# Kernel optimization log

Hardware: AMD Instinct MI355X
Metric: run time of the kernel (lower is better)

## Reference

```python
import math
import jax, jax.numpy as jnp
import numpy as np

B, L, T, D, H, SD = 8, 512, 512, 768, 12, 5


def setup_inputs() -> dict:
    key = jax.random.key(0)
    ks = jax.random.split(key, 16)
    s = 0.02
    return {
        "q": jax.random.normal(ks[0], (B, L, D), jnp.float32),
        "k": jax.random.normal(ks[1], (B, T, D), jnp.float32),
        "v": jax.random.normal(ks[2], (B, T, D), jnp.float32),
        "pairwise_locs": jax.random.normal(ks[3], (B, L, T, SD), jnp.float32),
        "key_padding_mask": jax.random.randint(ks[4], (B, T), 0, 2).astype(bool),
        "Wq": jax.random.normal(ks[5], (D, D), jnp.float32) * s,
        "bq": jnp.zeros((D,), jnp.float32),
        "Wk": jax.random.normal(ks[6], (D, D), jnp.float32) * s,
        "bk": jnp.zeros((D,), jnp.float32),
        "Wv": jax.random.normal(ks[7], (D, D), jnp.float32) * s,
        "bv": jnp.zeros((D,), jnp.float32),
        "Wl": jax.random.normal(ks[8], (D, H * (SD + 1)), jnp.float32) * s,
        "bl": jnp.zeros((H * (SD + 1),), jnp.float32),
        "Wf": jax.random.normal(ks[9], (D, D), jnp.float32) * s,
        "bf": jnp.zeros((D,), jnp.float32),
    }


def reference(q, k, v, pairwise_locs, key_padding_mask,
              Wq, bq, Wk, bk, Wv, bv, Wl, bl, Wf, bf):
    b, l, d = q.shape
    t = k.shape[1]
    sd = pairwise_locs.shape[-1]
    h = Wl.shape[1] // (sd + 1)          # spatial_multihead=True -> h == n_head
    dh = d // h

    # projections -> [h, b, seq, dh]
    qh = (q @ Wq + bq).reshape(b, l, h, dh).transpose(2, 0, 1, 3)
    kh = (k @ Wk + bk).reshape(b, t, h, dh).transpose(2, 0, 1, 3)
    vh = (v @ Wv + bv).reshape(b, t, h, dh).transpose(2, 0, 1, 3)

    attn = jnp.einsum('hblk,hbtk->hblt', qh, kh) / math.sqrt(dh)

    # language-conditioned spatial weights from residual (= q input)
    sw = (q @ Wl + bl).reshape(b, l, h, sd + 1).transpose(2, 0, 1, 3)  # [h,b,l,sd+1]
    spatial_bias = sw[..., :1]
    spatial_w = sw[..., 1:]
    loc_attn = jax.nn.sigmoid(
        jnp.einsum('hbld,bltd->hblt', spatial_w, pairwise_locs) + spatial_bias)

    mask = key_padding_mask[None, :, None, :]          # [1,b,1,t]
    attn = jnp.where(mask, -jnp.inf, attn)
    loc_attn = jnp.where(mask, 0.0, loc_attn)

    fused_attn = jax.nn.softmax(jnp.log(jnp.clip(loc_attn, 1e-6)) + attn, axis=3)

    out = jnp.einsum('hblt,hbtv->hblv', fused_attn, vh)
    out = out.transpose(1, 2, 0, 3).reshape(b, l, d)
    out = out @ Wf + bf
    return (out, fused_attn)
```

## Files before the change

kernel.cpp:

```cpp
#include <hip/hip_runtime.h>
#include <hip/hip_bf16.h>

#define B_ 8
#define L_ 512
#define T_ 512
#define D_ 768
#define H_ 12
#define DH_ 64
#define SD_ 5
#define NSW_ 72
#define K2_ 1536
#define K3_ 2304

typedef __attribute__((ext_vector_type(8))) short bf16x8;
typedef __attribute__((ext_vector_type(4))) float f32x4;
typedef unsigned short ushort_t;

__device__ __forceinline__ unsigned short f2bf(float x) {
    union { __hip_bfloat16 h; unsigned short u; } cv;
    cv.h = __float2bfloat16(x);
    return cv.u;
}
__device__ __forceinline__ float bf2f(unsigned short u) {
    union { unsigned short u; __hip_bfloat16 h; } cv;
    cv.u = u;
    return __bfloat162float(cv.h);
}

__device__ __forceinline__ void gload_lds16(const void* g, void* l) {
    __builtin_amdgcn_global_load_lds((const __attribute__((address_space(1))) void*)g,
                                     (__attribute__((address_space(3))) void*)l,
                                     16, 0, 0);
}

__global__ __launch_bounds__(256) void asplit_kernel(
    const float* __restrict__ q, const float* __restrict__ k, const float* __restrict__ v,
    short* __restrict__ q2, short* __restrict__ k2, short* __restrict__ v2)
{
    const int z = blockIdx.z;
    const float* A = (z == 0) ? q : (z == 1) ? k : v;
    short* O = (z == 0) ? q2 : (z == 1) ? k2 : v2;
    const int col = blockIdx.x * 256 + threadIdx.x;
    const int m   = blockIdx.y;
    if (col >= D_) return;
    const float a = A[(size_t)m * D_ + col];
    const unsigned short hi = f2bf(a);
    const unsigned short lo = f2bf(a - bf2f(hi));
    O[(size_t)m * K2_ + col]       = (short)hi;
    O[(size_t)m * K2_ + D_ + col]  = (short)lo;
}

__global__ __launch_bounds__(256) void wsplit_kernel(
    const float* __restrict__ Wq, const float* __restrict__ Wk,
    const float* __restrict__ Wv, const float* __restrict__ Wl,
    const float* __restrict__ Wf,
    short* __restrict__ WqT3, short* __restrict__ WkT3, short* __restrict__ WvT3,
    short* __restrict__ WlT3, short* __restrict__ WfT3)
{
    const int z = blockIdx.z;
    const float* W; short* O; int Nw, Npad;
    if (z == 0)      { W = Wq; O = WqT3; Nw = D_;   Npad = 768; }
    else if (z == 1) { W = Wk; O = WkT3; Nw = D_;   Npad = 768; }
    else if (z == 2) { W = Wv; O = WvT3; Nw = D_;   Npad = 768; }
    else if (z == 3) { W = Wl; O = WlT3; Nw = NSW_; Npad = 128; }
    else             { W = Wf; O = WfT3; Nw = D_;   Npad = 768; }

    const int k0 = blockIdx.x * 64;
    const int n0 = blockIdx.y * 64;
    if (n0 >= Npad) return;

    __shared__ float sm[64][65];
    const int c  = threadIdx.x & 63;
    const int r4 = threadIdx.x >> 6;

#pragma unroll
    for (int i = 0; i < 16; i++) {
        const int r = i * 4 + r4;
        float val = 0.f;
        if (n0 + c < Nw) val = W[(size_t)(k0 + r) * Nw + n0 + c];
        sm[r][c] = val;
    }
    __syncthreads();

#pragma unroll
    for (int i = 0; i < 16; i++) {
        const int nl = i * 4 + r4;
        const int n  = n0 + nl;
        if (n >= Npad) continue;
        const float v = (n < Nw) ? sm[c][nl] : 0.f;
        const unsigned short hi = f2bf(v);
        const unsigned short lo = f2bf(v - bf2f(hi));
        const size_t rb = (size_t)n * K3_;
        O[rb + k0 + c]        = (short)hi;
        O[rb + 768 + k0 + c]  = (short)lo;
        O[rb + 1536 + k0 + c] = (short)hi;
    }
}

__global__ __launch_bounds__(256) void mfma_gemm(
    const short* __restrict__ q2, const short* __restrict__ k2, const short* __restrict__ v2,
    const short* __restrict__ WqT3, const short* __restrict__ WkT3,
    const short* __restrict__ WvT3, const short* __restrict__ WlT3,
    const short* __restrict__ WfT3,
    const float* __restrict__ bq, const float* __restrict__ bk,
    const float* __restrict__ bv, const float* __restrict__ bl,
    const float* __restrict__ bf,
    const short* __restrict__ outp2,
    ushort_t* __restrict__ qs2a, ushort_t* __restrict__ ks2a, ushort_t* __restrict__ vt2,
    float* __restrict__ swv, float* __restrict__ outf,
    int zoff)
{
    const int nwg   = gridDim.x * gridDim.y * gridDim.z;
    const int flat  = blockIdx.x + gridDim.x * (blockIdx.y + gridDim.y * blockIdx.z);
    const int flat2 = (flat & 7) * (nwg >> 3) + (flat >> 3);
    const int bxg   = flat2 % 6;
    const int rem   = flat2 / 6;
    const int byg   = rem & 31;
    const int bzg   = rem >> 5;

    const int z = zoff + bzg;
    const short* A2; const short* WT3; const float* bias;
    if (z == 0)      { A2 = q2;    WT3 = WqT3; bias = bq; }
    else if (z == 1) { A2 = k2;    WT3 = WkT3; bias = bk; }
    else if (z == 2) { A2 = v2;    WT3 = WvT3; bias = bv; }
    else if (z == 3) { A2 = q2;    WT3 = WlT3; bias = bl; }
    else             { A2 = outp2; WT3 = WfT3; bias = bf; }

    if (z == 3 && bxg != 0) return;

    const int m0 = byg * 128;
    const int n0 = bxg * 128;

    __shared__ __align__(16) short As[2][128 * 64];
    __shared__ __align__(16) short Bs[2][128 * 64];

    const int tid  = threadIdx.x;
    const int lane = tid & 63;
    const int wv_  = tid >> 6;
    const int wm   = (wv_ & 1) << 6;
    const int wn   = (wv_ >> 1) << 6;
    const int l15  = lane & 15;
    const int quad = lane >> 4;

    f32x4 acc[4][4] = {};

    const int NT = K3_ / 64;

    auto stage = [&](int buf, int kb) {
        const int akb = (kb < 768) ? kb : kb - 768;
#pragma unroll
        for (int j = 0; j < 4; j++) {
            const int i = tid + 256 * j;
            const int r = i >> 3, c = i & 7, gc = c ^ (r & 7);
            gload_lds16(A2 + (size_t)(m0 + r) * K2_ + akb + gc * 8, &As[buf][i * 8]);
        }
#pragma unroll
        for (int j = 0; j < 4; j++) {
            const int i = tid + 256 * j;
            const int r = i >> 3, c = i & 7, gc = c ^ (r & 7);
            gload_lds16(WT3 + (size_t)(n0 + r) * K3_ + kb + gc * 8, &Bs[buf][i * 8]);
        }
    };

    stage(0, 0);
    stage(1, 64);

    int cur = 0;
    for (int t = 0; t < NT; ++t) {
        asm volatile("s_waitcnt vmcnt(8)" ::: "memory");
        __builtin_amdgcn_s_barrier();

        bf16x8 af[2][4], bfr[2][4];
#pragma unroll
        for (int tt = 0; tt < 4; tt++) {
            const int ar = wm + tt * 16 + l15;
            const int br = wn + tt * 16 + l15;
            af[0][tt]  = *(const bf16x8*)&As[cur][ar * 64 + (quad ^ (ar & 7)) * 8];
            bfr[0][tt] = *(const bf16x8*)&Bs[cur][br * 64 + (quad ^ (br & 7)) * 8];
        }
        __builtin_amdgcn_sched_barrier(0);
#pragma unroll
        for (int tt = 0; tt < 4; tt++) {
            const int ar = wm + tt * 16 + l15;
            const int br = wn + tt * 16 + l15;
            af[1][tt]  = *(const bf16x8*)&As[cur][ar * 64 + ((4 + quad) ^ (ar & 7)) * 8];
            bfr[1][tt] = *(const bf16x8*)&Bs[cur][br * 64 + ((4 + quad) ^ (br & 7)) * 8];
        }
        __builtin_amdgcn_sched_barrier(0);

        asm volatile("s_waitcnt lgkmcnt(8)" ::: "memory");
        __builtin_amdgcn_sched_barrier(0);
        __builtin_amdgcn_s_setprio(1);
#pragma unroll
        for (int mt = 0; mt < 4; mt++)
#pragma unroll
            for (int nt = 0; nt < 4; nt++)
                acc[mt][nt] = __builtin_amdgcn_mfma_f32_16x16x32_bf16(
                    af[0][mt], bfr[0][nt], acc[mt][nt], 0, 0, 0);
        __builtin_amdgcn_s_setprio(0);

        asm volatile("s_waitcnt lgkmcnt(0)" ::: "memory");
        __builtin_amdgcn_sched_barrier(0);
        __builtin_amdgcn_s_barrier();

        const int kb2 = (t + 2 < NT) ? (t + 2) * 64 : 0;
        stage(cur, kb2);
        __builtin_amdgcn_sched_barrier(0);

        __builtin_amdgcn_s_setprio(1);
#pragma unroll
        for (int mt = 0; mt < 4; mt++)
#pragma unroll
            for (int nt = 0; nt < 4; nt++)
                acc[mt][nt] = __builtin_amdgcn_mfma_f32_16x16x32_bf16(
                    af[1][mt], bfr[1][nt], acc[mt][nt], 0, 0, 0);
        __builtin_amdgcn_s_setprio(0);
        cur ^= 1;
    }
    asm volatile("s_waitcnt vmcnt(0)" ::: "memory");

    if (z <= 2) {
        ushort_t* dst = (z == 0) ? qs2a : (z == 1) ? ks2a : vt2;
#pragma unroll
        for (int nt = 0; nt < 4; nt++) {
            const int col = n0 + wn + nt * 16 + l15;
            const int hh = col >> 6, dd = col & 63;
            const float bvv = bias[col];
#pragma unroll
            for (int mt = 0; mt < 4; mt++) {
                const int rowb = m0 + wm + mt * 16 + quad * 4;
                if (z < 2) {
#pragma unroll
                    for (int r = 0; r < 4; r++) {
                        const int gr = rowb + r;
                        const int bb = gr >> 9, ll = gr & 511;
                        const float x = acc[mt][nt][r] + bvv;
                        const ushort_t hi = f2bf(x);
                        const ushort_t lo = f2bf(x - bf2f(hi));
                        const size_t base = (((size_t)hh * B_ + bb) * 512 + ll) * 128 + dd;
                        dst[base]      = hi;
                        dst[base + 64] = lo;
                    }
                } else {
                    const int bb = rowb >> 9, tt = rowb & 511;
                    ushort_t hi4[4], lo4[4];
#pragma unroll
                    for (int r = 0; r < 4; r++) {
                        const float x = acc[mt][nt][r] + bvv;
                        hi4[r] = f2bf(x);
                        lo4[r] = f2bf(x - bf2f(hi4[r]));
                    }
                    const size_t base = (((size_t)hh * B_ + bb) * 128 + dd) * 512 + tt;
                    *(ushort4*)&dst[base]            = *(ushort4*)hi4;
                    *(ushort4*)&dst[base + 64 * 512] = *(ushort4*)lo4;
                }
            }
        }
    } else if (z == 3) {
#pragma unroll
        for (int nt = 0; nt < 4; nt++) {
            const int col = n0 + wn + nt * 16 + l15;
            if (col >= NSW_) continue;
            const float bvv = bias[col];
#pragma unroll
            for (int mt = 0; mt < 4; mt++) {
                const int row = m0 + wm + mt * 16 + quad * 4;
#pragma unroll
                for (int r = 0; r < 4; r++)
                    swv[(size_t)(row + r) * NSW_ + col] = acc[mt][nt][r] + bvv;
            }
        }
    } else {
#pragma unroll
        for (int nt = 0; nt < 4; nt++) {
            const int col = n0 + wn + nt * 16 + l15;
            const float bvv = bias[col];
#pragma unroll
            for (int mt = 0; mt < 4; mt++) {
                const int row = m0 + wm + mt * 16 + quad * 4;
#pragma unroll
                for (int r = 0; r < 4; r++)
                    outf[(size_t)(row + r) * D_ + col] = acc[mt][nt][r] + bvv;
            }
        }
    }
}

__global__ __launch_bounds__(256) void sig_kernel(
    const float* __restrict__ ploc, const float* __restrict__ swv,
    const int* __restrict__ maskp, _Float16* __restrict__ sig16)
{
    const int b = blockIdx.y;
    const int l = blockIdx.x;
    const int tid = threadIdx.x;

    __shared__ float pls[512 * 5];
    __shared__ float sws[72];
    __shared__ int   msk[512];

    const float* src = ploc + (size_t)(b * 512 + l) * 512 * 5;
    for (int i = tid; i < 640; i += 256)
        *(float4*)&pls[i * 4] = *(const float4*)(src + i * 4);
    if (tid < 72) sws[tid] = swv[(size_t)(b * 512 + l) * NSW_ + tid];
    for (int i = tid; i < 512; i += 256) msk[i] = maskp[b * 512 + i];
    __syncthreads();

    for (int e = tid; e < H_ * 512; e += 256) {
        const int t  = e & 511;
        const int hh = e >> 9;
        float s = sws[hh * 6];
#pragma unroll
        for (int d = 0; d < SD_; d++) s += sws[hh * 6 + 1 + d] * pls[t * 5 + d];
        const float sig = msk[t] ? 0.f : fmaxf(1.f / (1.f + __expf(-s)), 1e-6f);
        sig16[(((size_t)hh * B_ + b) * 512 + l) * 512 + t] = (_Float16)sig;
    }
}

__global__ __launch_bounds__(256) void attn_kernel(
    const ushort_t* __restrict__ qs2, const ushort_t* __restrict__ ks2,
    const ushort_t* __restrict__ vt2, const _Float16* __restrict__ sig16,
    float* __restrict__ fused, ushort_t* __restrict__ outp2,
    float* __restrict__ sums)
{
    const int flat  = blockIdx.x + 8 * (blockIdx.y + 8 * blockIdx.z);
    const int flat2 = (flat & 7) * 96 + (flat >> 3);
    const int h  = flat2 / 64;
    const int b  = (flat2 >> 3) & 7;
    const int l0 = (flat2 & 7) << 6;

    const int hb = h * B_ + b;
    const int tid  = threadIdx.x;
    const int lane = tid & 63;
    const int wv   = tid >> 6;
    const int l15  = lane & 15;
    const int quad = lane >> 4;

    __shared__ __align__(16) ushort_t ks[2][64 * 128];
    __shared__ __align__(16) ushort_t vts[128 * 64];
    __shared__ __align__(16) ushort_t ps[64 * 152];
    __shared__ float ssb[4 * 64];
    __shared__ float ssum[64];

    bf16x8 qreg[4][4];
    {
        const ushort_t* qb = qs2 + ((size_t)hb * 512 + l0) * 128;
#pragma unroll
        for (int mt = 0; mt < 4; mt++) {
            const ushort_t* qr = qb + (size_t)(mt * 16 + l15) * 128 + quad * 8;
            qreg[mt][0] = *(const bf16x8*)(qr);
            qreg[mt][1] = *(const bf16x8*)(qr + 32);
            qreg[mt][2] = *(const bf16x8*)(qr + 64);
            qreg[mt][3] = *(const bf16x8*)(qr + 96);
        }
    }

    float pacc = 0.f;
    f32x4 accpv[4] = {};

    auto stageK = [&](int buf, int t0s) {
        const size_t kbase = ((size_t)hb * 512 + t0s) * 128;
#pragma unroll
        for (int j = 0; j < 4; j++) {
            const int i = tid + 256 * j;
            const int r = i >> 4, c = i & 15, gc = c ^ (r & 7);
            gload_lds16(ks2 + kbase + r * 128 + gc * 8, &ks[buf][i * 8]);
        }
    };
    auto stageV = [&](int t0s) {
        const size_t vbase = (size_t)hb * 128 * 512;
#pragma unroll
        for (int j = 0; j < 4; j++) {
            const int i = tid + 256 * j;
            const int r = i >> 3, c = i & 7, gc = c ^ (r & 7);
            gload_lds16(vt2 + vbase + (size_t)r * 512 + t0s + gc * 8, &vts[i * 8]);
        }
    };

    stageK(0, 0);

#pragma unroll 1
    for (int it = 0; it < 8; ++it) {
        const int t0  = it << 6;
        const int cur = it & 1;
        if (it == 0) asm volatile("s_waitcnt vmcnt(0)" ::: "memory");
        else         asm volatile("s_waitcnt vmcnt(4)" ::: "memory");
        __builtin_amdgcn_sched_barrier(0);
        __builtin_amdgcn_s_barrier();

        float sigv[4][4];
        {
            const _Float16* sgp = sig16 + (((size_t)hb * 512 + l0) * 512) + t0 + wv * 16 + l15;
#pragma unroll
            for (int mt = 0; mt < 4; mt++)
#pragma unroll
                for (int r2 = 0; r2 < 4; r2++)
                    sigv[mt][r2] = (float)sgp[(size_t)(mt * 16 + quad * 4 + r2) * 512];
        }
        __builtin_amdgcn_sched_barrier(0);
        stageV(t0);
        stageK(cur ^ 1, (it < 7) ? t0 + 64 : 0);
        __builtin_amdgcn_sched_barrier(0);

        f32x4 acq[4] = {};
        {
            const int trow = wv * 16 + l15;
            const int tsw  = trow & 7;
            const bf16x8 bk0 = *(const bf16x8*)&ks[cur][trow * 128 + ((0  + quad) ^ tsw) * 8];
            const bf16x8 bk1 = *(const bf16x8*)&ks[cur][trow * 128 + ((4  + quad) ^ tsw) * 8];
            const bf16x8 bk2 = *(const bf16x8*)&ks[cur][trow * 128 + ((8  + quad) ^ tsw) * 8];
            const bf16x8 bk3 = *(const bf16x8*)&ks[cur][trow * 128 + ((12 + quad) ^ tsw) * 8];
            __builtin_amdgcn_s_setprio(1);
#pragma unroll
            for (int mt = 0; mt < 4; mt++) {
                f32x4 a = acq[mt];
                a = __builtin_amdgcn_mfma_f32_16x16x32_bf16(qreg[mt][0], bk0, a, 0, 0, 0);
                a = __builtin_amdgcn_mfma_f32_16x16x32_bf16(qreg[mt][1], bk1, a, 0, 0, 0);
                a = __builtin_amdgcn_mfma_f32_16x16x32_bf16(qreg[mt][0], bk2, a, 0, 0, 0);
                a = __builtin_amdgcn_mfma_f32_16x16x32_bf16(qreg[mt][1], bk3, a, 0, 0, 0);
                a = __builtin_amdgcn_mfma_f32_16x16x32_bf16(qreg[mt][2], bk0, a, 0, 0, 0);
                a = __builtin_amdgcn_mfma_f32_16x16x32_bf16(qreg[mt][3], bk1, a, 0, 0, 0);
                acq[mt] = a;
            }
            __builtin_amdgcn_s_setprio(0);
        }

        {
            const int tcol = wv * 16 + l15;
#pragma unroll
            for (int mt = 0; mt < 4; mt++)
#pragma unroll
                for (int r2 = 0; r2 < 4; r2++) {
                    const int lrow = mt * 16 + quad * 4 + r2;
                    const float p  = sigv[mt][r2] * __expf(acq[mt][r2] * 0.125f);
                    const ushort_t hi = f2bf(p);
                    const ushort_t lo = f2bf(p - bf2f(hi));
                    ps[lrow * 152 + tcol]      = hi;
                    ps[lrow * 152 + 64 + tcol] = lo;
                }
        }
        asm volatile("s_waitcnt lgkmcnt(0) vmcnt(4)" ::: "memory");
        __builtin_amdgcn_sched_barrier(0);
        __builtin_amdgcn_s_barrier();

        {
            const int row = tid >> 2, c4 = tid & 3;
            const bf16x8 h0 = *(const bf16x8*)&ps[row * 152 + c4 * 16];
            const bf16x8 h1 = *(const bf16x8*)&ps[row * 152 + c4 * 16 + 8];
            const bf16x8 g0 = *(const bf16x8*)&ps[row * 152 + 64 + c4 * 16];
            const bf16x8 g1 = *(const bf16x8*)&ps[row * 152 + 64 + c4 * 16 + 8];
            float vbuf[16];
            float s = 0.f;
#pragma unroll
            for (int jj = 0; jj < 8; jj++) {
                vbuf[jj]     = bf2f((ushort_t)h0[jj]) + bf2f((ushort_t)g0[jj]);
                vbuf[8 + jj] = bf2f((ushort_t)h1[jj]) + bf2f((ushort_t)g1[jj]);
                s += vbuf[jj] + vbuf[8 + jj];
            }
            pacc += s;
            float* dstf = fused + ((size_t)hb * 512 + l0 + row) * 512 + t0 + c4 * 16;
#pragma unroll
            for (int jj = 0; jj < 4; jj++)
                *(float4*)(dstf + jj * 4) = *(float4*)&vbuf[jj * 4];
        }

        {
            const int vrh = wv * 16 + l15;
            const int vrl = 64 + vrh;
            const int swh = vrh & 7, swl = vrl & 7;
            const bf16x8 bh0 = *(const bf16x8*)&vts[vrh * 64 + ((0 + quad) ^ swh) * 8];
            const bf16x8 bh1 = *(const bf16x8*)&vts[vrh * 64 + ((4 + quad) ^ swh) * 8];
            const bf16x8 bl0 = *(const bf16x8*)&vts[vrl * 64 + ((0 + quad) ^ swl) * 8];
            const bf16x8 bl1 = *(const bf16x8*)&vts[vrl * 64 + ((4 + quad) ^ swl) * 8];
            __builtin_amdgcn_s_setprio(1);
#pragma unroll
            for (int mt = 0; mt < 4; mt++) {
                const int prow = mt * 16 + l15;
                const bf16x8 ph0 = *(const bf16x8*)&ps[prow * 152 + 0  + quad * 8];
                const bf16x8 ph1 = *(const bf16x8*)&ps[prow * 152 + 32 + quad * 8];
                const bf16x8 pl0 = *(const bf16x8*)&ps[prow * 152 + 64 + quad * 8];
                const bf16x8 pl1 = *(const bf16x8*)&ps[prow * 152 + 96 + quad * 8];
                f32x4 a = accpv[mt];
                a = __builtin_amdgcn_mfma_f32_16x16x32_bf16(ph0, bh0, a, 0, 0, 0);
                a = __builtin_amdgcn_mfma_f32_16x16x32_bf16(ph1, bh1, a, 0, 0, 0);
                a = __builtin_amdgcn_mfma_f32_16x16x32_bf16(ph0, bl0, a, 0, 0, 0);
                a = __builtin_amdgcn_mfma_f32_16x16x32_bf16(ph1, bl1, a, 0, 0, 0);
                a = __builtin_amdgcn_mfma_f32_16x16x32_bf16(pl0, bh0, a, 0, 0, 0);
                a = __builtin_amdgcn_mfma_f32_16x16x32_bf16(pl1, bh1, a, 0, 0, 0);
                accpv[mt] = a;
            }
            __builtin_amdgcn_s_setprio(0);
        }
    }
    asm volatile("s_waitcnt vmcnt(0)" ::: "memory");

    __syncthreads();
    ssb[(tid & 3) * 64 + (tid >> 2)] = pacc;
    __syncthreads();
    if (tid < 64) {
        const float s = ssb[tid] + ssb[64 + tid] + ssb[128 + tid] + ssb[192 + tid];
        ssum[tid] = s;
        sums[(size_t)hb * 512 + l0 + tid] = s;
    }
    __syncthreads();

#pragma unroll
    for (int mt = 0; mt < 4; mt++)
#pragma unroll
        for (int r2 = 0; r2 < 4; r2++) {
            const int lrow = mt * 16 + quad * 4 + r2;
            const float val = accpv[mt][r2] / ssum[lrow];
            const ushort_t hi = f2bf(val);
            const ushort_t lo = f2bf(val - bf2f(hi));
            const size_t obase = ((size_t)(b * 512 + l0 + lrow)) * K2_ + h * 64 + wv * 16 + l15;
            outp2[obase]       = hi;
            outp2[obase + D_]  = lo;
        }
}

__global__ __launch_bounds__(256) void norm_kernel(
    float* __restrict__ fused, const float* __restrict__ sums)
{
    const int gi = blockIdx.x * 256 + threadIdx.x;
    float4* f4 = (float4*)fused;
    float4 v = f4[gi];
    const float inv = 1.f / sums[gi >> 7];
    v.x *= inv; v.y *= inv; v.z *= inv; v.w *= inv;
    f4[gi] = v;
}

extern "C" void kernel_launch(void* const* d_in, const int* in_sizes, int n_in,
                              void* d_out, int out_size, void* d_ws, size_t ws_size,
                              hipStream_t stream) {
    const float* q    = (const float*)d_in[0];
    const float* k    = (const float*)d_in[1];
    const float* v    = (const float*)d_in[2];
    const float* ploc = (const float*)d_in[3];
    const int*   mask = (const int*)  d_in[4];
    const float* Wq   = (const float*)d_in[5];
    const float* bq   = (const float*)d_in[6];
    const float* Wk   = (const float*)d_in[7];
    const float* bk   = (const float*)d_in[8];
    const float* Wv   = (const float*)d_in[9];
    const float* bv   = (const float*)d_in[10];
    const float* Wl   = (const float*)d_in[11];
    const float* bl   = (const float*)d_in[12];
    const float* Wf   = (const float*)d_in[13];
    const float* bf   = (const float*)d_in[14];

    char* base = (char*)d_ws;
    short*    q2    = (short*)(base + 0);
    short*    k2    = (short*)(base + 12582912);
    short*    v2    = (short*)(base + 25165824);
    short*    WqT3  = (short*)(base + 37748736);
    short*    WkT3  = (short*)(base + 41287680);
    short*    WvT3  = (short*)(base + 44826624);
    short*    WlT3  = (short*)(base + 48365568);
    _Float16* sig16 = (_Float16*)(base + 0);
    short*    WfT3  = (short*)(base + 50331648);
    ushort_t* qs2a  = (ushort_t*)(base + 53870592);
    ushort_t* ks2a  = (ushort_t*)(base + 66453504);
    ushort_t* vt2   = (ushort_t*)(base + 79036416);
    float*    swv   = (float*)(base + 91619328);
    float*    sums  = (float*)(base + 92798976);
    short*    outp2 = (short*)(base + 92995584);

    float* out   = (float*)d_out;
    float* fused = out + (size_t)4096 * D_;

    asplit_kernel<<<dim3(3, 4096, 3), 256, 0, stream>>>(q, k, v, q2, k2, v2);
    wsplit_kernel<<<dim3(12, 12, 5), 256, 0, stream>>>(
        Wq, Wk, Wv, Wl, Wf, WqT3, WkT3, WvT3, WlT3, WfT3);

    mfma_gemm<<<dim3(6, 32, 4), 256, 0, stream>>>(
        q2, k2, v2, WqT3, WkT3, WvT3, WlT3, WfT3,
        bq, bk, bv, bl, bf, outp2, qs2a, ks2a, vt2, swv, out, 0);

    sig_kernel<<<dim3(512, 8), 256, 0, stream>>>(ploc, swv, mask, sig16);

    attn_kernel<<<dim3(8, 8, 12), 256, 0, stream>>>(
        qs2a, ks2a, vt2, sig16, fused, (ushort_t*)outp2, sums);

    norm_kernel<<<dim3(24576), 256, 0, stream>>>(fused, sums);

    mfma_gemm<<<dim3(6, 32, 1), 256, 0, stream>>>(
        q2, k2, v2, WqT3, WkT3, WvT3, WlT3, WfT3,
        bq, bk, bv, bl, bf, outp2, qs2a, ks2a, vt2, swv, out, 4);
}
```

Before: 461.9 us.

## Stage hi/lo halves together in split-bf16 GEMM to drop tripled weight copy

```diff
diff --git a/kernel.cpp b/kernel.cpp
--- a/kernel.cpp
+++ b/kernel.cpp
@@ -10,7 +10,6 @@
 #define SD_ 5
 #define NSW_ 72
 #define K2_ 1536
-#define K3_ 2304
 
 typedef __attribute__((ext_vector_type(8))) short bf16x8;
 typedef __attribute__((ext_vector_type(4))) float f32x4;
@@ -54,16 +53,16 @@
     const float* __restrict__ Wq, const float* __restrict__ Wk,
     const float* __restrict__ Wv, const float* __restrict__ Wl,
     const float* __restrict__ Wf,
-    short* __restrict__ WqT3, short* __restrict__ WkT3, short* __restrict__ WvT3,
-    short* __restrict__ WlT3, short* __restrict__ WfT3)
+    short* __restrict__ WqT2, short* __restrict__ WkT2, short* __restrict__ WvT2,
+    short* __restrict__ WlT2, short* __restrict__ WfT2)
 {
     const int z = blockIdx.z;
     const float* W; short* O; int Nw, Npad;
-    if (z == 0)      { W = Wq; O = WqT3; Nw = D_;   Npad = 768; }
-    else if (z == 1) { W = Wk; O = WkT3; Nw = D_;   Npad = 768; }
-    else if (z == 2) { W = Wv; O = WvT3; Nw = D_;   Npad = 768; }
-    else if (z == 3) { W = Wl; O = WlT3; Nw = NSW_; Npad = 128; }
-    else             { W = Wf; O = WfT3; Nw = D_;   Npad = 768; }
+    if (z == 0)      { W = Wq; O = WqT2; Nw = D_;   Npad = 768; }
+    else if (z == 1) { W = Wk; O = WkT2; Nw = D_;   Npad = 768; }
+    else if (z == 2) { W = Wv; O = WvT2; Nw = D_;   Npad = 768; }
+    else if (z == 3) { W = Wl; O = WlT2; Nw = NSW_; Npad = 128; }
+    else             { W = Wf; O = WfT2; Nw = D_;   Npad = 768; }
 
     const int k0 = blockIdx.x * 64;
     const int n0 = blockIdx.y * 64;
@@ -90,18 +89,17 @@
         const float v = (n < Nw) ? sm[c][nl] : 0.f;
         const unsigned short hi = f2bf(v);
         const unsigned short lo = f2bf(v - bf2f(hi));
-        const size_t rb = (size_t)n * K3_;
+        const size_t rb = (size_t)n * K2_;
         O[rb + k0 + c]        = (short)hi;
         O[rb + 768 + k0 + c]  = (short)lo;
-        O[rb + 1536 + k0 + c] = (short)hi;
     }
 }
 
 __global__ __launch_bounds__(256) void mfma_gemm(
     const short* __restrict__ q2, const short* __restrict__ k2, const short* __restrict__ v2,
-    const short* __restrict__ WqT3, const short* __restrict__ WkT3,
-    const short* __restrict__ WvT3, const short* __restrict__ WlT3,
-    const short* __restrict__ WfT3,
+    const short* __restrict__ WqT2, const short* __restrict__ WkT2,
+    const short* __restrict__ WvT2, const short* __restrict__ WlT2,
+    const short* __restrict__ WfT2,
     const float* __restrict__ bq, const float* __restrict__ bk,
     const float* __restrict__ bv, const float* __restrict__ bl,
     const float* __restrict__ bf,
@@ -119,12 +117,12 @@
     const int bzg   = rem >> 5;
 
     const int z = zoff + bzg;
-    const short* A2; const short* WT3; const float* bias;
-    if (z == 0)      { A2 = q2;    WT3 = WqT3; bias = bq; }
-    else if (z == 1) { A2 = k2;    WT3 = WkT3; bias = bk; }
-    else if (z == 2) { A2 = v2;    WT3 = WvT3; bias = bv; }
-    else if (z == 3) { A2 = q2;    WT3 = WlT3; bias = bl; }
-    else             { A2 = outp2; WT3 = WfT3; bias = bf; }
+    const short* A2; const short* WT2; const float* bias;
+    if (z == 0)      { A2 = q2;    WT2 = WqT2; bias = bq; }
+    else if (z == 1) { A2 = k2;    WT2 = WkT2; bias = bk; }
+    else if (z == 2) { A2 = v2;    WT2 = WvT2; bias = bv; }
+    else if (z == 3) { A2 = q2;    WT2 = WlT2; bias = bl; }
+    else             { A2 = outp2; WT2 = WfT2; bias = bf; }
 
     if (z == 3 && bxg != 0) return;
 
@@ -144,77 +142,80 @@
 
     f32x4 acc[4][4] = {};
 
-    const int NT = K3_ / 64;
+    const int NT = 768 / 32;
 
     auto stage = [&](int buf, int kb) {
-        const int akb = (kb < 768) ? kb : kb - 768;
 #pragma unroll
         for (int j = 0; j < 4; j++) {
             const int i = tid + 256 * j;
-            const int r = i >> 3, c = i & 7, gc = c ^ (r & 7);
-            gload_lds16(A2 + (size_t)(m0 + r) * K2_ + akb + gc * 8, &As[buf][i * 8]);
+            const int r = i >> 3, c = i & 7, g = c ^ (r & 7);
+            const int col = kb + g * 8 + (g >> 2) * 736;
+            gload_lds16(A2 + (size_t)(m0 + r) * K2_ + col, &As[buf][i * 8]);
         }
 #pragma unroll
         for (int j = 0; j < 4; j++) {
             const int i = tid + 256 * j;
-            const int r = i >> 3, c = i & 7, gc = c ^ (r & 7);
-            gload_lds16(WT3 + (size_t)(n0 + r) * K3_ + kb + gc * 8, &Bs[buf][i * 8]);
+            const int r = i >> 3, c = i & 7, g = c ^ (r & 7);
+            const int col = kb + g * 8 + (g >> 2) * 736;
+            gload_lds16(WT2 + (size_t)(n0 + r) * K2_ + col, &Bs[buf][i * 8]);
         }
     };
 
     stage(0, 0);
-    stage(1, 64);
+    stage(1, 32);
 
     int cur = 0;
     for (int t = 0; t < NT; ++t) {
         asm volatile("s_waitcnt vmcnt(8)" ::: "memory");
         __builtin_amdgcn_s_barrier();
 
-        bf16x8 af[2][4], bfr[2][4];
+        bf16x8 afh[4], bfh[4], afl[4], bfl[4];
 #pragma unroll
         for (int tt = 0; tt < 4; tt++) {
             const int ar = wm + tt * 16 + l15;
             const int br = wn + tt * 16 + l15;
-            af[0][tt]  = *(const bf16x8*)&As[cur][ar * 64 + (quad ^ (ar & 7)) * 8];
-            bfr[0][tt] = *(const bf16x8*)&Bs[cur][br * 64 + (quad ^ (br & 7)) * 8];
+            afh[tt] = *(const bf16x8*)&As[cur][ar * 64 + (quad ^ (ar & 7)) * 8];
+            bfh[tt] = *(const bf16x8*)&Bs[cur][br * 64 + (quad ^ (br & 7)) * 8];
         }
         __builtin_amdgcn_sched_barrier(0);
 #pragma unroll
         for (int tt = 0; tt < 4; tt++) {
             const int ar = wm + tt * 16 + l15;
             const int br = wn + tt * 16 + l15;
-            af[1][tt]  = *(const bf16x8*)&As[cur][ar * 64 + ((4 + quad) ^ (ar & 7)) * 8];
-            bfr[1][tt] = *(const bf16x8*)&Bs[cur][br * 64 + ((4 + quad) ^ (br & 7)) * 8];
+            afl[tt] = *(const bf16x8*)&As[cur][ar * 64 + ((4 + quad) ^ (ar & 7)) * 8];
+            bfl[tt] = *(const bf16x8*)&Bs[cur][br * 64 + ((4 + quad) ^ (br & 7)) * 8];
         }
         __builtin_amdgcn_sched_barrier(0);
 
         asm volatile("s_waitcnt lgkmcnt(8)" ::: "memory");
         __builtin_amdgcn_sched_barrier(0);
-        __builtin_amdgcn_s_setprio(1);
 #pragma unroll
         for (int mt = 0; mt < 4; mt++)
 #pragma unroll
             for (int nt = 0; nt < 4; nt++)
                 acc[mt][nt] = __builtin_amdgcn_mfma_f32_16x16x32_bf16(
-                    af[0][mt], bfr[0][nt], acc[mt][nt], 0, 0, 0);
-        __builtin_amdgcn_s_setprio(0);
+                    afh[mt], bfh[nt], acc[mt][nt], 0, 0, 0);
 
         asm volatile("s_waitcnt lgkmcnt(0)" ::: "memory");
         __builtin_amdgcn_sched_barrier(0);
         __builtin_amdgcn_s_barrier();
 
-        const int kb2 = (t + 2 < NT) ? (t + 2) * 64 : 0;
+        const int kb2 = (t + 2 < NT) ? (t + 2) * 32 : 0;
         stage(cur, kb2);
         __builtin_amdgcn_sched_barrier(0);
 
-        __builtin_amdgcn_s_setprio(1);
 #pragma unroll
         for (int mt = 0; mt < 4; mt++)
 #pragma unroll
             for (int nt = 0; nt < 4; nt++)
                 acc[mt][nt] = __builtin_amdgcn_mfma_f32_16x16x32_bf16(
-                    af[1][mt], bfr[1][nt], acc[mt][nt], 0, 0, 0);
-        __builtin_amdgcn_s_setprio(0);
+                    afh[mt], bfl[nt], acc[mt][nt], 0, 0, 0);
+#pragma unroll
+        for (int mt = 0; mt < 4; mt++)
+#pragma unroll
+            for (int nt = 0; nt < 4; nt++)
+                acc[mt][nt] = __builtin_amdgcn_mfma_f32_16x16x32_bf16(
+                    afl[mt], bfh[nt], acc[mt][nt], 0, 0, 0);
         cur ^= 1;
     }
     asm volatile("s_waitcnt vmcnt(0)" ::: "memory");
@@ -409,7 +410,6 @@
             const bf16x8 bk1 = *(const bf16x8*)&ks[cur][trow * 128 + ((4  + quad) ^ tsw) * 8];
             const bf16x8 bk2 = *(const bf16x8*)&ks[cur][trow * 128 + ((8  + quad) ^ tsw) * 8];
             const bf16x8 bk3 = *(const bf16x8*)&ks[cur][trow * 128 + ((12 + quad) ^ tsw) * 8];
-            __builtin_amdgcn_s_setprio(1);
 #pragma unroll
             for (int mt = 0; mt < 4; mt++) {
                 f32x4 a = acq[mt];
@@ -421,7 +421,6 @@
                 a = __builtin_amdgcn_mfma_f32_16x16x32_bf16(qreg[mt][3], bk1, a, 0, 0, 0);
                 acq[mt] = a;
             }
-            __builtin_amdgcn_s_setprio(0);
         }
 
         {
@@ -471,7 +470,6 @@
             const bf16x8 bh1 = *(const bf16x8*)&vts[vrh * 64 + ((4 + quad) ^ swh) * 8];
             const bf16x8 bl0 = *(const bf16x8*)&vts[vrl * 64 + ((0 + quad) ^ swl) * 8];
             const bf16x8 bl1 = *(const bf16x8*)&vts[vrl * 64 + ((4 + quad) ^ swl) * 8];
-            __builtin_amdgcn_s_setprio(1);
 #pragma unroll
             for (int mt = 0; mt < 4; mt++) {
                 const int prow = mt * 16 + l15;
@@ -488,7 +486,6 @@
                 a = __builtin_amdgcn_mfma_f32_16x16x32_bf16(pl1, bh1, a, 0, 0, 0);
                 accpv[mt] = a;
             }
-            __builtin_amdgcn_s_setprio(0);
         }
     }
     asm volatile("s_waitcnt vmcnt(0)" ::: "memory");
@@ -551,12 +548,12 @@
     short*    q2    = (short*)(base + 0);
     short*    k2    = (short*)(base + 12582912);
     short*    v2    = (short*)(base + 25165824);
-    short*    WqT3  = (short*)(base + 37748736);
-    short*    WkT3  = (short*)(base + 41287680);
-    short*    WvT3  = (short*)(base + 44826624);
-    short*    WlT3  = (short*)(base + 48365568);
+    short*    WqT2  = (short*)(base + 37748736);
+    short*    WkT2  = (short*)(base + 41287680);
+    short*    WvT2  = (short*)(base + 44826624);
+    short*    WlT2  = (short*)(base + 48365568);
     _Float16* sig16 = (_Float16*)(base + 0);
-    short*    WfT3  = (short*)(base + 50331648);
+    short*    WfT2  = (short*)(base + 50331648);
     ushort_t* qs2a  = (ushort_t*)(base + 53870592);
     ushort_t* ks2a  = (ushort_t*)(base + 66453504);
     ushort_t* vt2   = (ushort_t*)(base + 79036416);
@@ -569,10 +566,10 @@
 
     asplit_kernel<<<dim3(3, 4096, 3), 256, 0, stream>>>(q, k, v, q2, k2, v2);
     wsplit_kernel<<<dim3(12, 12, 5), 256, 0, stream>>>(
-        Wq, Wk, Wv, Wl, Wf, WqT3, WkT3, WvT3, WlT3, WfT3);
+        Wq, Wk, Wv, Wl, Wf, WqT2, WkT2, WvT2, WlT2, WfT2);
 
     mfma_gemm<<<dim3(6, 32, 4), 256, 0, stream>>>(
-        q2, k2, v2, WqT3, WkT3, WvT3, WlT3, WfT3,
+        q2, k2, v2, WqT2, WkT2, WvT2, WlT2, WfT2,
         bq, bk, bv, bl, bf, outp2, qs2a, ks2a, vt2, swv, out, 0);
 
     sig_kernel<<<dim3(512, 8), 256, 0, stream>>>(ploc, swv, mask, sig16);
@@ -583,6 +580,6 @@
     norm_kernel<<<dim3(24576), 256, 0, stream>>>(fused, sums);
 
     mfma_gemm<<<dim3(6, 32, 1), 256, 0, stream>>>(
-        q2, k2, v2, WqT3, WkT3, WvT3, WlT3, WfT3,
+        q2, k2, v2, WqT2, WkT2, WvT2, WlT2, WfT2,
         bq, bk, bv, bl, bf, outp2, qs2a, ks2a, vt2, swv, out, 4);
 }
```

Result: faster. 439.9 us (-4.8%).
